# Kernel optimization log

Measured on AMD Instinct MI355X. Metric: run time of the kernel, lower is better.

## Reference

```python
import jax, jax.numpy as jnp
import numpy as np

N = 50000      # nodes
E = 1600000    # edges (avg degree 32)
C = 48         # num_classes
S = 10         # num_steps


def setup_inputs() -> dict:
    key = jax.random.key(0)
    k1, k2, k3, k4 = jax.random.split(key, 4)
    edge_index = jax.random.randint(k1, (2, E), 0, N)
    edge_attr = jax.random.uniform(k2, (E,), dtype=jnp.float32)  # positive edge weights
    target = jax.random.randint(k3, (N,), 0, C)
    bound = 1.0 / np.sqrt(S)  # uniform(size, weight) init from PyG
    weight = jax.random.uniform(k4, (C, S), minval=-bound, maxval=bound, dtype=jnp.float32)
    return {"edge_index": edge_index, "edge_attr": edge_attr, "target": target, "weight": weight}


def reference(edge_index, edge_attr, target, weight):
    """Adaptive-diffusion random walk: propagate one-hot class indicators
    through a row-normalized weighted transition matrix for S steps and
    combine step-wise landing distributions with learned weight[c, s]."""
    row, col = edge_index[0], edge_index[1]
    # Row-normalize edge weights -> random-walk transition probabilities
    deg = jax.ops.segment_sum(edge_attr, row, num_segments=N)          # [N]
    norm = edge_attr / jnp.clip(deg, 1e-12)[row]                        # [E]
    h0 = jax.nn.one_hot(target, C, dtype=weight.dtype)                  # [N, C]

    def step(h, w_s):
        # message = P^T-style aggregation: scatter src features to dst
        h_new = jax.ops.segment_sum(norm[:, None] * h[row], col, num_segments=N)  # [N, C]
        return h_new, h_new * w_s  # w_s: [C], per-class step coefficient

    _, contribs = jax.lax.scan(step, h0, weight.T)  # contribs: [S, N, C]
    return contribs.sum(0)                          # [N, C]
```

## Files before the change

### kernel.cpp

```cpp
#include <hip/hip_runtime.h>
#include <hip/hip_fp16.h>

#define NN 50000
#define NE 1600000
#define NC 48
#define NS 10
#define PAD 88
#define PADN 50176

#define NBUCK 392
#define NB2   784
#define CAP   4608
#define EPB   2048
#define EPT   2

typedef __attribute__((ext_vector_type(8))) _Float16 half8;

__global__ __launch_bounds__(1024) void bin_kernel(const int* __restrict__ row,
        const int* __restrict__ col, const float* __restrict__ attr,
        int* __restrict__ bcur, uint2* __restrict__ bin, unsigned int* __restrict__ rbin) {
    __shared__ int hcnt[NB2];
    __shared__ int hbase[NB2];
    __shared__ int lofs[NB2];
    __shared__ int sc[1024];
    __shared__ uint2 stageC[EPB];
    __shared__ unsigned int stageR[EPB];
    int tid = threadIdx.x;
    if (tid < NB2) hcnt[tid] = 0;
    __syncthreads();
    int base = blockIdx.x * EPB;
    int ntot = min(EPB, NE - base);
    unsigned int rec[EPT];
    int cv[EPT];
    #pragma unroll
    for (int k = 0; k < EPT; ++k) {
        int e = base + k * 1024 + tid;
        if (e < NE) {
            int r = row[e], c = col[e];
            unsigned int iq = (unsigned int)rintf(attr[e] * 65535.0f);
            rec[k] = (iq << 16) | (unsigned int)r;
            cv[k] = c;
            atomicAdd(&hcnt[c >> 7], 1);
            atomicAdd(&hcnt[NBUCK + (r >> 7)], 1);
        } else {
            cv[k] = -1;
        }
    }
    __syncthreads();
    if (tid < NB2) hbase[tid] = atomicAdd(&bcur[tid], hcnt[tid]);
    sc[tid] = (tid < NB2) ? hcnt[tid] : 0;
    __syncthreads();
    for (int off = 1; off < 1024; off <<= 1) {
        int t = (tid >= off) ? sc[tid - off] : 0;
        __syncthreads();
        sc[tid] += t;
        __syncthreads();
    }
    if (tid < NB2) {
        lofs[tid] = sc[tid] - hcnt[tid];
        hcnt[tid] = 0;
    }
    __syncthreads();
    #pragma unroll
    for (int k = 0; k < EPT; ++k) {
        if (cv[k] >= 0) {
            int b = cv[k] >> 7;
            int rk = atomicAdd(&hcnt[b], 1);
            stageC[lofs[b] + rk] = make_uint2(rec[k], (unsigned int)cv[k]);
            int b2 = NBUCK + ((rec[k] & 0xffffu) >> 7);
            int rk2 = atomicAdd(&hcnt[b2], 1);
            stageR[lofs[b2] + rk2 - ntot] = rec[k];
        }
    }
    __syncthreads();
    for (int i = tid; i < ntot; i += 1024) {
        uint2 rc = stageC[i];
        int b = (int)(rc.y >> 7);
        bin[(size_t)b * CAP + hbase[b] + (i - lofs[b])] = rc;
    }
    for (int i = tid; i < ntot; i += 1024) {
        unsigned int rr = stageR[i];
        int b2 = NBUCK + ((rr & 0xffffu) >> 7);
        rbin[(size_t)(b2 - NBUCK) * CAP + hbase[b2] + (i + ntot - lofs[b2])] = rr;
    }
}

__global__ __launch_bounds__(1024) void degrdeg_kernel(const int* __restrict__ bcur,
        const unsigned int* __restrict__ rbin, const int* __restrict__ target,
        float* __restrict__ rdeg, int2* __restrict__ tq) {
    __shared__ unsigned int acc[128];
    int rb = blockIdx.x;
    if (threadIdx.x < 128) acc[threadIdx.x] = 0;
    __syncthreads();
    int n = bcur[NBUCK + rb];
    const unsigned int* rp = rbin + (size_t)rb * CAP;
    for (int i = threadIdx.x; i < n; i += 1024) {
        unsigned int rr = rp[i];
        atomicAdd(&acc[rr & 127], rr >> 16);
    }
    __syncthreads();
    if (threadIdx.x < 128) {
        int v = (rb << 7) + threadIdx.x;
        if (v < NN) {
            float rd = 65535.0f / fmaxf((float)acc[threadIdx.x], 1.0f);
            rdeg[v] = rd;
            tq[v] = make_int2(target[v], __float_as_int(rd));
        }
    }
}

__global__ __launch_bounds__(1024) void place_kernel(const int* __restrict__ bcur,
        const uint2* __restrict__ bin, unsigned int* __restrict__ edges,
        int* __restrict__ cnt) {
    __shared__ int ccnt[128];
    int b = blockIdx.x;
    if (threadIdx.x < 128) ccnt[threadIdx.x] = 0;
    __syncthreads();
    int n = bcur[b];
    const uint2* rp = bin + (size_t)b * CAP;
    for (int i = threadIdx.x; i < n; i += 1024) {
        uint2 r = rp[i];
        int c = (int)r.y;
        int pos = atomicAdd(&ccnt[c & 127], 1);
        edges[(size_t)c * PAD + pos] = r.x;
    }
    __syncthreads();
    if (threadIdx.x < 128) {
        int c = (b << 7) + threadIdx.x;
        if (c < NN) cnt[c] = ccnt[threadIdx.x];
    }
}

__global__ __launch_bounds__(256) void step1_kernel(const int* __restrict__ cnt,
        const unsigned int* __restrict__ edges, const int2* __restrict__ tq,
        const float* __restrict__ rdeg, const float* __restrict__ weight,
        _Float16* __restrict__ p_new, float* __restrict__ out) {
    int idx = blockIdx.x * blockDim.x + threadIdx.x;
    if (idx >= NN * 6) return;
    int v = idx / 6;
    int q = idx - v * 6;
    int n = cnt[v];
    const unsigned int* ep = edges + (size_t)v * PAD;
    int c0 = 8 * q;
    float a[8] = {0.f, 0.f, 0.f, 0.f, 0.f, 0.f, 0.f, 0.f};
    int i = 0;
    for (; i + 4 <= n; i += 4) {
        uint4 pa = *reinterpret_cast<const uint4*>(ep + i);
        int2 t0 = tq[pa.x & 0xffffu];
        int2 t1 = tq[pa.y & 0xffffu];
        int2 t2 = tq[pa.z & 0xffffu];
        int2 t3 = tq[pa.w & 0xffffu];
        float w0 = (float)(pa.x >> 16) * __int_as_float(t0.y);
        float w1 = (float)(pa.y >> 16) * __int_as_float(t1.y);
        float w2 = (float)(pa.z >> 16) * __int_as_float(t2.y);
        float w3 = (float)(pa.w >> 16) * __int_as_float(t3.y);
        int b0 = t0.x - c0, b1 = t1.x - c0, b2 = t2.x - c0, b3 = t3.x - c0;
        #pragma unroll
        for (int j = 0; j < 8; ++j) {
            a[j] += (b0 == j) ? w0 : 0.f;
            a[j] += (b1 == j) ? w1 : 0.f;
            a[j] += (b2 == j) ? w2 : 0.f;
            a[j] += (b3 == j) ? w3 : 0.f;
        }
    }
    for (; i < n; ++i) {
        unsigned int w_ = ep[i];
        int2 t0 = tq[w_ & 0xffffu];
        float w0 = (float)(w_ >> 16) * __int_as_float(t0.y);
        int b0 = t0.x - c0;
        #pragma unroll
        for (int j = 0; j < 8; ++j) a[j] += (b0 == j) ? w0 : 0.f;
    }
    #pragma unroll
    for (int j = 0; j < 8; ++j) a[j] *= (1.0f / 65535.0f);

    size_t off = (size_t)v * NC + c0;
    float w[8];
    #pragma unroll
    for (int j = 0; j < 8; ++j) w[j] = weight[(c0 + j) * NS + 0];
    *reinterpret_cast<float4*>(out + off) =
        make_float4(a[0] * w[0], a[1] * w[1], a[2] * w[2], a[3] * w[3]);
    *reinterpret_cast<float4*>(out + off + 4) =
        make_float4(a[4] * w[4], a[5] * w[5], a[6] * w[6], a[7] * w[7]);
    float rd = rdeg[v];
    half8 ph;
    #pragma unroll
    for (int j = 0; j < 8; ++j) ph[j] = (_Float16)(a[j] * rd);
    *reinterpret_cast<half8*>(p_new + off) = ph;
}

__device__ __forceinline__ const half8* prow(unsigned int w_, const char* pb) {
    return reinterpret_cast<const half8*>(pb + (w_ & 0xffffu) * (NC * 2));
}

__device__ __forceinline__ void fma8(float* a, float wv, half8 g) {
    #pragma unroll
    for (int j = 0; j < 8; ++j) a[j] += wv * (float)g[j];
}

template <bool LAST>
__global__ __launch_bounds__(256) void gather_kernel(const int* __restrict__ cnt,
        const unsigned int* __restrict__ edges, const float* __restrict__ rdeg,
        const _Float16* __restrict__ p, _Float16* __restrict__ p_new,
        const float* __restrict__ weight, int t, float* __restrict__ out) {
    int idx = blockIdx.x * blockDim.x + threadIdx.x;
    if (idx >= NN * 6) return;
    int v = idx / 6;
    int q = idx - v * 6;
    int n = cnt[v];
    const unsigned int* ep = edges + (size_t)v * PAD;
    const char* pb = (const char*)p + q * 16;
    float a[8] = {0.f, 0.f, 0.f, 0.f, 0.f, 0.f, 0.f, 0.f};
    int i = 0;
    for (; i + 8 <= n; i += 8) {
        uint4 pa = *reinterpret_cast<const uint4*>(ep + i);
        uint4 pc = *reinterpret_cast<const uint4*>(ep + i + 4);
        half8 g0 = *prow(pa.x, pb);
        half8 g1 = *prow(pa.y, pb);
        half8 g2 = *prow(pa.z, pb);
        half8 g3 = *prow(pa.w, pb);
        half8 g4 = *prow(pc.x, pb);
        half8 g5 = *prow(pc.y, pb);
        half8 g6 = *prow(pc.z, pb);
        half8 g7 = *prow(pc.w, pb);
        const float sc = 1.0f / 65535.0f;
        fma8(a, (float)(pa.x >> 16) * sc, g0);
        fma8(a, (float)(pa.y >> 16) * sc, g1);
        fma8(a, (float)(pa.z >> 16) * sc, g2);
        fma8(a, (float)(pa.w >> 16) * sc, g3);
        fma8(a, (float)(pc.x >> 16) * sc, g4);
        fma8(a, (float)(pc.y >> 16) * sc, g5);
        fma8(a, (float)(pc.z >> 16) * sc, g6);
        fma8(a, (float)(pc.w >> 16) * sc, g7);
    }
    if (i + 4 <= n) {
        uint4 pa = *reinterpret_cast<const uint4*>(ep + i);
        half8 g0 = *prow(pa.x, pb);
        half8 g1 = *prow(pa.y, pb);
        half8 g2 = *prow(pa.z, pb);
        half8 g3 = *prow(pa.w, pb);
        const float sc = 1.0f / 65535.0f;
        fma8(a, (float)(pa.x >> 16) * sc, g0);
        fma8(a, (float)(pa.y >> 16) * sc, g1);
        fma8(a, (float)(pa.z >> 16) * sc, g2);
        fma8(a, (float)(pa.w >> 16) * sc, g3);
        i += 4;
    }
    for (; i < n; ++i) {
        unsigned int w_ = ep[i];
        fma8(a, (float)(w_ >> 16) * (1.0f / 65535.0f), *prow(w_, pb));
    }

    size_t off = (size_t)v * NC + q * 8;
    int c0 = 8 * q;
    float w[8];
    #pragma unroll
    for (int j = 0; j < 8; ++j) w[j] = weight[(c0 + j) * NS + (t - 1)];
    float* op = out + off;
    float4 o0 = *reinterpret_cast<float4*>(op);
    float4 o1 = *reinterpret_cast<float4*>(op + 4);
    o0.x += a[0] * w[0]; o0.y += a[1] * w[1]; o0.z += a[2] * w[2]; o0.w += a[3] * w[3];
    o1.x += a[4] * w[4]; o1.y += a[5] * w[5]; o1.z += a[6] * w[6]; o1.w += a[7] * w[7];
    *reinterpret_cast<float4*>(op) = o0;
    *reinterpret_cast<float4*>(op + 4) = o1;
    if (!LAST) {
        float rd = rdeg[v];
        half8 ph;
        #pragma unroll
        for (int j = 0; j < 8; ++j) ph[j] = (_Float16)(a[j] * rd);
        *reinterpret_cast<half8*>(p_new + off) = ph;
    }
}

extern "C" void kernel_launch(void* const* d_in, const int* in_sizes, int n_in,
                              void* d_out, int out_size, void* d_ws, size_t ws_size,
                              hipStream_t stream) {
    const int*   edge_index = (const int*)d_in[0];
    const float* edge_attr  = (const float*)d_in[1];
    const int*   target     = (const int*)d_in[2];
    const float* weight     = (const float*)d_in[3];
    float* out = (float*)d_out;

    const int* row = edge_index;
    const int* col = edge_index + NE;

    float*        rdeg  = (float*)d_ws;
    int*          bcur  = (int*)(rdeg + PADN);
    int*          cnt   = bcur + 1024;
    int2*         tq    = (int2*)(cnt + PADN);
    unsigned int* edges = (unsigned int*)(tq + NN);
    unsigned int* rbin  = edges;
    uint2*        bin   = (uint2*)(edges + (size_t)NN * PAD);
    _Float16*     pA    = (_Float16*)((char*)bin + (size_t)NBUCK * CAP * sizeof(uint2)
                                      - (size_t)2 * NN * NC * sizeof(_Float16));
    _Float16*     pB    = pA + (size_t)NN * NC;

    hipMemsetAsync(bcur, 0, 1024 * sizeof(int), stream);

    bin_kernel<<<(NE + EPB - 1) / EPB, 1024, 0, stream>>>(row, col, edge_attr,
            bcur, bin, rbin);
    degrdeg_kernel<<<NBUCK, 1024, 0, stream>>>(bcur, rbin, target, rdeg, tq);
    place_kernel<<<NBUCK, 1024, 0, stream>>>(bcur, bin, edges, cnt);

    const int gblocks = (NN * 6 + 255) / 256;
    _Float16* p = pA;
    _Float16* p_new = pB;
    step1_kernel<<<gblocks, 256, 0, stream>>>(cnt, edges, tq, rdeg, weight, p, out);
    for (int t = 2; t <= NS - 1; ++t) {
        gather_kernel<false><<<gblocks, 256, 0, stream>>>(cnt, edges, rdeg, p, p_new,
                                                          weight, t, out);
        _Float16* tmp = p; p = p_new; p_new = tmp;
    }
    gather_kernel<true><<<gblocks, 256, 0, stream>>>(cnt, edges, rdeg, p, p_new,
                                                     weight, NS, out);
}
```

Measured before the change: 383.9 us.

## Fuse diffusion steps into one cooperative kernel with grid syncs

Replaces the per-step launches of step1 and gather kernels with a single cooperative kernel that loops over all steps and uses grid-wide syncs between them. Output accumulation stays in registers and is written once at the end, which removes the per-step read-modify-write of the fp32 output. Falls back to the old multi-launch path if occupancy is too low for all blocks to be co-resident. The gain depends on 1172 blocks of 256 fitting on the device at once. Grid sync cost, plus lower occupancy from the launch-bounds hint, may offset the saved launch overhead.

Result: no change. 387.9 us (+1.1%).

```diff
diff --git a/kernel.cpp b/kernel.cpp
--- a/kernel.cpp
+++ b/kernel.cpp
@@ -1,5 +1,8 @@
 #include <hip/hip_runtime.h>
 #include <hip/hip_fp16.h>
+#include <hip/hip_cooperative_groups.h>
+
+namespace cg = cooperative_groups;
 
 #define NN 50000
 #define NE 1600000
@@ -128,6 +131,141 @@
     if (threadIdx.x < 128) {
         int c = (b << 7) + threadIdx.x;
         if (c < NN) cnt[c] = ccnt[threadIdx.x];
+    }
+}
+
+__device__ __forceinline__ const half8* prow(unsigned int w_, const char* pb) {
+    return reinterpret_cast<const half8*>(pb + (w_ & 0xffffu) * (NC * 2));
+}
+
+__device__ __forceinline__ void fma8(float* a, float wv, half8 g) {
+    #pragma unroll
+    for (int j = 0; j < 8; ++j) a[j] += wv * (float)g[j];
+}
+
+__global__ __launch_bounds__(256, 6) void fused_steps(const int* __restrict__ cnt,
+        const unsigned int* __restrict__ edges, const int2* __restrict__ tq,
+        const float* __restrict__ rdeg, const float* __restrict__ weight,
+        _Float16* __restrict__ pA, _Float16* __restrict__ pB, float* __restrict__ out) {
+    cg::grid_group gg = cg::this_grid();
+    int idx = blockIdx.x * blockDim.x + threadIdx.x;
+    const bool valid = idx < NN * 6;
+    int v = idx / 6;
+    int q = idx - v * 6;
+    if (!valid) { v = 0; q = 0; }
+    const int n = valid ? cnt[v] : 0;
+    const unsigned int* ep = edges + (size_t)v * PAD;
+    const int c0 = 8 * q;
+    const float rd = valid ? rdeg[v] : 0.f;
+    const size_t off = (size_t)v * NC + c0;
+    const float sc = 1.0f / 65535.0f;
+    float out8[8] = {0.f, 0.f, 0.f, 0.f, 0.f, 0.f, 0.f, 0.f};
+
+    _Float16* cur = pA;
+    _Float16* nxt = pB;
+
+    if (valid) {
+        float a[8] = {0.f, 0.f, 0.f, 0.f, 0.f, 0.f, 0.f, 0.f};
+        int i = 0;
+        for (; i + 4 <= n; i += 4) {
+            uint4 pa = *reinterpret_cast<const uint4*>(ep + i);
+            int2 t0 = tq[pa.x & 0xffffu];
+            int2 t1 = tq[pa.y & 0xffffu];
+            int2 t2 = tq[pa.z & 0xffffu];
+            int2 t3 = tq[pa.w & 0xffffu];
+            float w0 = (float)(pa.x >> 16) * __int_as_float(t0.y);
+            float w1 = (float)(pa.y >> 16) * __int_as_float(t1.y);
+            float w2 = (float)(pa.z >> 16) * __int_as_float(t2.y);
+            float w3 = (float)(pa.w >> 16) * __int_as_float(t3.y);
+            int b0 = t0.x - c0, b1 = t1.x - c0, b2 = t2.x - c0, b3 = t3.x - c0;
+            #pragma unroll
+            for (int j = 0; j < 8; ++j) {
+                a[j] += (b0 == j) ? w0 : 0.f;
+                a[j] += (b1 == j) ? w1 : 0.f;
+                a[j] += (b2 == j) ? w2 : 0.f;
+                a[j] += (b3 == j) ? w3 : 0.f;
+            }
+        }
+        for (; i < n; ++i) {
+            unsigned int w_ = ep[i];
+            int2 t0 = tq[w_ & 0xffffu];
+            float w0 = (float)(w_ >> 16) * __int_as_float(t0.y);
+            int b0 = t0.x - c0;
+            #pragma unroll
+            for (int j = 0; j < 8; ++j) a[j] += (b0 == j) ? w0 : 0.f;
+        }
+        #pragma unroll
+        for (int j = 0; j < 8; ++j) a[j] *= sc;
+        #pragma unroll
+        for (int j = 0; j < 8; ++j) out8[j] = a[j] * weight[(c0 + j) * NS + 0];
+        half8 ph;
+        #pragma unroll
+        for (int j = 0; j < 8; ++j) ph[j] = (_Float16)(a[j] * rd);
+        *reinterpret_cast<half8*>(cur + off) = ph;
+    }
+    gg.sync();
+
+    for (int t = 2; t <= NS; ++t) {
+        if (valid) {
+            const char* pb = (const char*)cur + q * 16;
+            float a[8] = {0.f, 0.f, 0.f, 0.f, 0.f, 0.f, 0.f, 0.f};
+            int i = 0;
+            for (; i + 8 <= n; i += 8) {
+                uint4 pa = *reinterpret_cast<const uint4*>(ep + i);
+                uint4 pc = *reinterpret_cast<const uint4*>(ep + i + 4);
+                half8 g0 = *prow(pa.x, pb);
+                half8 g1 = *prow(pa.y, pb);
+                half8 g2 = *prow(pa.z, pb);
+                half8 g3 = *prow(pa.w, pb);
+                half8 g4 = *prow(pc.x, pb);
+                half8 g5 = *prow(pc.y, pb);
+                half8 g6 = *prow(pc.z, pb);
+                half8 g7 = *prow(pc.w, pb);
+                fma8(a, (float)(pa.x >> 16) * sc, g0);
+                fma8(a, (float)(pa.y >> 16) * sc, g1);
+                fma8(a, (float)(pa.z >> 16) * sc, g2);
+                fma8(a, (float)(pa.w >> 16) * sc, g3);
+                fma8(a, (float)(pc.x >> 16) * sc, g4);
+                fma8(a, (float)(pc.y >> 16) * sc, g5);
+                fma8(a, (float)(pc.z >> 16) * sc, g6);
+                fma8(a, (float)(pc.w >> 16) * sc, g7);
+            }
+            if (i + 4 <= n) {
+                uint4 pa = *reinterpret_cast<const uint4*>(ep + i);
+                half8 g0 = *prow(pa.x, pb);
+                half8 g1 = *prow(pa.y, pb);
+                half8 g2 = *prow(pa.z, pb);
+                half8 g3 = *prow(pa.w, pb);
+                fma8(a, (float)(pa.x >> 16) * sc, g0);
+                fma8(a, (float)(pa.y >> 16) * sc, g1);
+                fma8(a, (float)(pa.z >> 16) * sc, g2);
+                fma8(a, (float)(pa.w >> 16) * sc, g3);
+                i += 4;
+            }
+            for (; i < n; ++i) {
+                unsigned int w_ = ep[i];
+                fma8(a, (float)(w_ >> 16) * sc, *prow(w_, pb));
+            }
+            #pragma unroll
+            for (int j = 0; j < 8; ++j) out8[j] += a[j] * weight[(c0 + j) * NS + (t - 1)];
+            if (t < NS) {
+                half8 ph;
+                #pragma unroll
+                for (int j = 0; j < 8; ++j) ph[j] = (_Float16)(a[j] * rd);
+                *reinterpret_cast<half8*>(nxt + off) = ph;
+            }
+        }
+        if (t < NS) {
+            gg.sync();
+            _Float16* tm = cur; cur = nxt; nxt = tm;
+        }
+    }
+
+    if (valid) {
+        *reinterpret_cast<float4*>(out + off) =
+            make_float4(out8[0], out8[1], out8[2], out8[3]);
+        *reinterpret_cast<float4*>(out + off + 4) =
+            make_float4(out8[4], out8[5], out8[6], out8[7]);
     }
 }
 
@@ -189,15 +327,6 @@
     *reinterpret_cast<half8*>(p_new + off) = ph;
 }
 
-__device__ __forceinline__ const half8* prow(unsigned int w_, const char* pb) {
-    return reinterpret_cast<const half8*>(pb + (w_ & 0xffffu) * (NC * 2));
-}
-
-__device__ __forceinline__ void fma8(float* a, float wv, half8 g) {
-    #pragma unroll
-    for (int j = 0; j < 8; ++j) a[j] += wv * (float)g[j];
-}
-
 template <bool LAST>
 __global__ __launch_bounds__(256) void gather_kernel(const int* __restrict__ cnt,
         const unsigned int* __restrict__ edges, const float* __restrict__ rdeg,
@@ -211,6 +340,7 @@
     const unsigned int* ep = edges + (size_t)v * PAD;
     const char* pb = (const char*)p + q * 16;
     float a[8] = {0.f, 0.f, 0.f, 0.f, 0.f, 0.f, 0.f, 0.f};
+    const float sc = 1.0f / 65535.0f;
     int i = 0;
     for (; i + 8 <= n; i += 8) {
         uint4 pa = *reinterpret_cast<const uint4*>(ep + i);
@@ -223,7 +353,6 @@
         half8 g5 = *prow(pc.y, pb);
         half8 g6 = *prow(pc.z, pb);
         half8 g7 = *prow(pc.w, pb);
-        const float sc = 1.0f / 65535.0f;
         fma8(a, (float)(pa.x >> 16) * sc, g0);
         fma8(a, (float)(pa.y >> 16) * sc, g1);
         fma8(a, (float)(pa.z >> 16) * sc, g2);
@@ -239,7 +368,6 @@
         half8 g1 = *prow(pa.y, pb);
         half8 g2 = *prow(pa.z, pb);
         half8 g3 = *prow(pa.w, pb);
-        const float sc = 1.0f / 65535.0f;
         fma8(a, (float)(pa.x >> 16) * sc, g0);
         fma8(a, (float)(pa.y >> 16) * sc, g1);
         fma8(a, (float)(pa.z >> 16) * sc, g2);
@@ -248,7 +376,7 @@
     }
     for (; i < n; ++i) {
         unsigned int w_ = ep[i];
-        fma8(a, (float)(w_ >> 16) * (1.0f / 65535.0f), *prow(w_, pb));
+        fma8(a, (float)(w_ >> 16) * sc, *prow(w_, pb));
     }
 
     size_t off = (size_t)v * NC + q * 8;
@@ -295,7 +423,7 @@
                                       - (size_t)2 * NN * NC * sizeof(_Float16));
     _Float16*     pB    = pA + (size_t)NN * NC;
 
-    hipMemsetAsync(bcur, 0, 1024 * sizeof(int), stream);
+    (void)hipMemsetAsync(bcur, 0, 1024 * sizeof(int), stream);
 
     bin_kernel<<<(NE + EPB - 1) / EPB, 1024, 0, stream>>>(row, col, edge_attr,
             bcur, bin, rbin);
@@ -303,14 +431,36 @@
     place_kernel<<<NBUCK, 1024, 0, stream>>>(bcur, bin, edges, cnt);
 
     const int gblocks = (NN * 6 + 255) / 256;
-    _Float16* p = pA;
-    _Float16* p_new = pB;
-    step1_kernel<<<gblocks, 256, 0, stream>>>(cnt, edges, tq, rdeg, weight, p, out);
-    for (int t = 2; t <= NS - 1; ++t) {
-        gather_kernel<false><<<gblocks, 256, 0, stream>>>(cnt, edges, rdeg, p, p_new,
-                                                          weight, t, out);
-        _Float16* tmp = p; p = p_new; p_new = tmp;
-    }
-    gather_kernel<true><<<gblocks, 256, 0, stream>>>(cnt, edges, rdeg, p, p_new,
-                                                     weight, NS, out);
-}
+
+    static int s_capacity = -2;
+    if (s_capacity == -2) {
+        int perCU = 0, nCU = 0, dev = 0;
+        hipError_t e0 = hipGetDevice(&dev);
+        hipError_t e1 = hipDeviceGetAttribute(&nCU, hipDeviceAttributeMultiprocessorCount, dev);
+        hipError_t e2 = hipOccupancyMaxActiveBlocksPerMultiprocessor(&perCU, fused_steps, 256, 0);
+        s_capacity = (e0 == hipSuccess && e1 == hipSuccess && e2 == hipSuccess)
+                         ? perCU * nCU : -1;
+    }
+
+    bool fused_ok = (s_capacity >= gblocks);
+    if (fused_ok) {
+        void* kargs[] = { (void*)&cnt, (void*)&edges, (void*)&tq, (void*)&rdeg,
+                          (void*)&weight, (void*)&pA, (void*)&pB, (void*)&out };
+        hipError_t le = hipLaunchCooperativeKernel((void*)fused_steps, dim3(gblocks),
+                                                   dim3(256), kargs, 0, stream);
+        if (le != hipSuccess) fused_ok = false;
+    }
+
+    if (!fused_ok) {
+        _Float16* p = pA;
+        _Float16* p_new = pB;
+        step1_kernel<<<gblocks, 256, 0, stream>>>(cnt, edges, tq, rdeg, weight, p, out);
+        for (int t = 2; t <= NS - 1; ++t) {
+            gather_kernel<false><<<gblocks, 256, 0, stream>>>(cnt, edges, rdeg, p, p_new,
+                                                              weight, t, out);
+            _Float16* tmp = p; p = p_new; p_new = tmp;
+        }
+        gather_kernel<true><<<gblocks, 256, 0, stream>>>(cnt, edges, rdeg, p, p_new,
+                                                         weight, NS, out);
+    }
+}
```

## Store all step states in fp16 and apply weights in a final combine kernel

Applied to the files above, without the earlier changes.

Each propagation step now writes only its fp16 normalized state into a separate slot of a stacked buffer. The per-step read-modify-write of the fp32 output is removed from the gather kernels. A new finish kernel reads all ten stored states, applies the per-class step weights, undoes the degree scaling, and writes the output once. This trades repeated fp32 output traffic for extra workspace, one more launch, and a final pass over ten fp16 arrays. It also places the new buffer after the bin region, which needs a larger workspace.

New measurement: 360.6 us. 1.06x faster.

```diff
diff --git a/kernel.cpp b/kernel.cpp
--- a/kernel.cpp
+++ b/kernel.cpp
@@ -131,10 +131,19 @@
     }
 }
 
+__device__ __forceinline__ const half8* prow(unsigned int w_, const char* pb) {
+    return reinterpret_cast<const half8*>(pb + (w_ & 0xffffu) * (NC * 2));
+}
+
+__device__ __forceinline__ void fma8(float* a, float wv, half8 g) {
+    #pragma unroll
+    for (int j = 0; j < 8; ++j) a[j] += wv * (float)g[j];
+}
+
+
 __global__ __launch_bounds__(256) void step1_kernel(const int* __restrict__ cnt,
         const unsigned int* __restrict__ edges, const int2* __restrict__ tq,
-        const float* __restrict__ rdeg, const float* __restrict__ weight,
-        _Float16* __restrict__ p_new, float* __restrict__ out) {
+        const float* __restrict__ rdeg, _Float16* __restrict__ p_new) {
     int idx = blockIdx.x * blockDim.x + threadIdx.x;
     if (idx >= NN * 6) return;
     int v = idx / 6;
@@ -171,38 +180,16 @@
         #pragma unroll
         for (int j = 0; j < 8; ++j) a[j] += (b0 == j) ? w0 : 0.f;
     }
-    #pragma unroll
-    for (int j = 0; j < 8; ++j) a[j] *= (1.0f / 65535.0f);
-
-    size_t off = (size_t)v * NC + c0;
-    float w[8];
-    #pragma unroll
-    for (int j = 0; j < 8; ++j) w[j] = weight[(c0 + j) * NS + 0];
-    *reinterpret_cast<float4*>(out + off) =
-        make_float4(a[0] * w[0], a[1] * w[1], a[2] * w[2], a[3] * w[3]);
-    *reinterpret_cast<float4*>(out + off + 4) =
-        make_float4(a[4] * w[4], a[5] * w[5], a[6] * w[6], a[7] * w[7]);
-    float rd = rdeg[v];
+    float rd = rdeg[v] * (1.0f / 65535.0f);
     half8 ph;
     #pragma unroll
     for (int j = 0; j < 8; ++j) ph[j] = (_Float16)(a[j] * rd);
-    *reinterpret_cast<half8*>(p_new + off) = ph;
-}
-
-__device__ __forceinline__ const half8* prow(unsigned int w_, const char* pb) {
-    return reinterpret_cast<const half8*>(pb + (w_ & 0xffffu) * (NC * 2));
-}
-
-__device__ __forceinline__ void fma8(float* a, float wv, half8 g) {
-    #pragma unroll
-    for (int j = 0; j < 8; ++j) a[j] += wv * (float)g[j];
-}
-
-template <bool LAST>
+    *reinterpret_cast<half8*>(p_new + (size_t)v * NC + c0) = ph;
+}
+
 __global__ __launch_bounds__(256) void gather_kernel(const int* __restrict__ cnt,
         const unsigned int* __restrict__ edges, const float* __restrict__ rdeg,
-        const _Float16* __restrict__ p, _Float16* __restrict__ p_new,
-        const float* __restrict__ weight, int t, float* __restrict__ out) {
+        const _Float16* __restrict__ p, _Float16* __restrict__ p_new) {
     int idx = blockIdx.x * blockDim.x + threadIdx.x;
     if (idx >= NN * 6) return;
     int v = idx / 6;
@@ -211,6 +198,7 @@
     const unsigned int* ep = edges + (size_t)v * PAD;
     const char* pb = (const char*)p + q * 16;
     float a[8] = {0.f, 0.f, 0.f, 0.f, 0.f, 0.f, 0.f, 0.f};
+    const float sc = 1.0f / 65535.0f;
     int i = 0;
     for (; i + 8 <= n; i += 8) {
         uint4 pa = *reinterpret_cast<const uint4*>(ep + i);
@@ -223,7 +211,6 @@
         half8 g5 = *prow(pc.y, pb);
         half8 g6 = *prow(pc.z, pb);
         half8 g7 = *prow(pc.w, pb);
-        const float sc = 1.0f / 65535.0f;
         fma8(a, (float)(pa.x >> 16) * sc, g0);
         fma8(a, (float)(pa.y >> 16) * sc, g1);
         fma8(a, (float)(pa.z >> 16) * sc, g2);
@@ -239,7 +226,6 @@
         half8 g1 = *prow(pa.y, pb);
         half8 g2 = *prow(pa.z, pb);
         half8 g3 = *prow(pa.w, pb);
-        const float sc = 1.0f / 65535.0f;
         fma8(a, (float)(pa.x >> 16) * sc, g0);
         fma8(a, (float)(pa.y >> 16) * sc, g1);
         fma8(a, (float)(pa.z >> 16) * sc, g2);
@@ -248,28 +234,38 @@
     }
     for (; i < n; ++i) {
         unsigned int w_ = ep[i];
-        fma8(a, (float)(w_ >> 16) * (1.0f / 65535.0f), *prow(w_, pb));
-    }
-
-    size_t off = (size_t)v * NC + q * 8;
+        fma8(a, (float)(w_ >> 16) * sc, *prow(w_, pb));
+    }
+
+    float rd = rdeg[v];
+    half8 ph;
+    #pragma unroll
+    for (int j = 0; j < 8; ++j) ph[j] = (_Float16)(a[j] * rd);
+    *reinterpret_cast<half8*>(p_new + (size_t)v * NC + q * 8) = ph;
+}
+
+__global__ __launch_bounds__(256) void finish_kernel(const float* __restrict__ rdeg,
+        const _Float16* __restrict__ pS0, const float* __restrict__ weight,
+        float* __restrict__ out) {
+    int idx = blockIdx.x * blockDim.x + threadIdx.x;
+    if (idx >= NN * 6) return;
+    int v = idx / 6;
+    int q = idx - v * 6;
     int c0 = 8 * q;
-    float w[8];
-    #pragma unroll
-    for (int j = 0; j < 8; ++j) w[j] = weight[(c0 + j) * NS + (t - 1)];
-    float* op = out + off;
-    float4 o0 = *reinterpret_cast<float4*>(op);
-    float4 o1 = *reinterpret_cast<float4*>(op + 4);
-    o0.x += a[0] * w[0]; o0.y += a[1] * w[1]; o0.z += a[2] * w[2]; o0.w += a[3] * w[3];
-    o1.x += a[4] * w[4]; o1.y += a[5] * w[5]; o1.z += a[6] * w[6]; o1.w += a[7] * w[7];
-    *reinterpret_cast<float4*>(op) = o0;
-    *reinterpret_cast<float4*>(op + 4) = o1;
-    if (!LAST) {
-        float rd = rdeg[v];
-        half8 ph;
+    size_t off = (size_t)v * NC + c0;
+    float out8[8] = {0.f, 0.f, 0.f, 0.f, 0.f, 0.f, 0.f, 0.f};
+    #pragma unroll
+    for (int s = 0; s < NS; ++s) {
+        half8 ph = *reinterpret_cast<const half8*>(pS0 + (size_t)s * (NN * NC) + off);
         #pragma unroll
-        for (int j = 0; j < 8; ++j) ph[j] = (_Float16)(a[j] * rd);
-        *reinterpret_cast<half8*>(p_new + off) = ph;
-    }
+        for (int j = 0; j < 8; ++j)
+            out8[j] += (float)ph[j] * weight[(c0 + j) * NS + s];
+    }
+    float hinv = 1.0f / rdeg[v];
+    *reinterpret_cast<float4*>(out + off) =
+        make_float4(out8[0] * hinv, out8[1] * hinv, out8[2] * hinv, out8[3] * hinv);
+    *reinterpret_cast<float4*>(out + off + 4) =
+        make_float4(out8[4] * hinv, out8[5] * hinv, out8[6] * hinv, out8[7] * hinv);
 }
 
 extern "C" void kernel_launch(void* const* d_in, const int* in_sizes, int n_in,
@@ -291,11 +287,10 @@
     unsigned int* edges = (unsigned int*)(tq + NN);
     unsigned int* rbin  = edges;
     uint2*        bin   = (uint2*)(edges + (size_t)NN * PAD);
-    _Float16*     pA    = (_Float16*)((char*)bin + (size_t)NBUCK * CAP * sizeof(uint2)
-                                      - (size_t)2 * NN * NC * sizeof(_Float16));
-    _Float16*     pB    = pA + (size_t)NN * NC;
-
-    hipMemsetAsync(bcur, 0, 1024 * sizeof(int), stream);
+    _Float16*     pS0   = (_Float16*)(bin + (size_t)NBUCK * CAP);
+    const size_t  PSTRIDE = (size_t)NN * NC;
+
+    (void)hipMemsetAsync(bcur, 0, 1024 * sizeof(int), stream);
 
     bin_kernel<<<(NE + EPB - 1) / EPB, 1024, 0, stream>>>(row, col, edge_attr,
             bcur, bin, rbin);
@@ -303,14 +298,10 @@
     place_kernel<<<NBUCK, 1024, 0, stream>>>(bcur, bin, edges, cnt);
 
     const int gblocks = (NN * 6 + 255) / 256;
-    _Float16* p = pA;
-    _Float16* p_new = pB;
-    step1_kernel<<<gblocks, 256, 0, stream>>>(cnt, edges, tq, rdeg, weight, p, out);
-    for (int t = 2; t <= NS - 1; ++t) {
-        gather_kernel<false><<<gblocks, 256, 0, stream>>>(cnt, edges, rdeg, p, p_new,
-                                                          weight, t, out);
-        _Float16* tmp = p; p = p_new; p_new = tmp;
-    }
-    gather_kernel<true><<<gblocks, 256, 0, stream>>>(cnt, edges, rdeg, p, p_new,
-                                                     weight, NS, out);
-}
+    step1_kernel<<<gblocks, 256, 0, stream>>>(cnt, edges, tq, rdeg, pS0);
+    for (int t = 2; t <= NS; ++t) {
+        gather_kernel<<<gblocks, 256, 0, stream>>>(cnt, edges, rdeg,
+                pS0 + (size_t)(t - 2) * PSTRIDE, pS0 + (size_t)(t - 1) * PSTRIDE);
+    }
+    finish_kernel<<<gblocks, 256, 0, stream>>>(rdeg, pS0, weight, out);
+}
```
